# Optimization experiments

Measured on AMD Instinct MI355X. Metric: run time of the kernel, lower is better.

The kernel has to match this reference:

```python
import jax, jax.numpy as jnp
import numpy as np

V, H, B, T = 100000, 512, 4096, 524288
EPS = 1e-5

def setup_inputs() -> dict:
    key = jax.random.key(0)
    ks = jax.random.split(key, 8)
    tokens = jax.random.randint(ks[0], (T,), 0, V, dtype=jnp.int32)
    seg_ids = jnp.sort(jax.random.randint(ks[1], (T,), 0, B, dtype=jnp.int32))
    t = jax.random.bernoulli(ks[2], 0.5, (B,)).astype(jnp.float32)
    emb = jax.random.normal(ks[3], (V, H), dtype=jnp.float32) * 0.1
    W1 = jax.random.normal(ks[4], (H, H), dtype=jnp.float32) * (1.0 / np.sqrt(H))
    b1 = jnp.zeros((H,), jnp.float32)
    gamma = jnp.ones((H,), jnp.float32)
    beta = jnp.zeros((H,), jnp.float32)
    w2 = jax.random.normal(ks[5], (H,), dtype=jnp.float32) * (1.0 / np.sqrt(H))
    b2 = jnp.zeros((), jnp.float32)
    return {"tokens": tokens, "seg_ids": seg_ids, "t": t, "emb": emb,
            "W1": W1, "b1": b1, "gamma": gamma, "beta": beta, "w2": w2, "b2": b2}

def reference(tokens, seg_ids, t, emb, W1, b1, gamma, beta, w2, b2):
    nb = t.shape[0]
    # fused gather + segment-mean (bag-of-words), replaces the per-sample loop
    gathered = emb[tokens]  # [T, H]
    sums = jax.ops.segment_sum(gathered, seg_ids, num_segments=nb)  # [B, H]
    counts = jax.ops.segment_sum(jnp.ones((tokens.shape[0],), jnp.float32), seg_ids, num_segments=nb)
    bow = sums / jnp.maximum(counts, 1.0)[:, None]  # [B, H]
    # Linear -> BatchNorm1d (training-mode batch stats, biased var) -> ReLU
    z = bow @ W1.T + b1  # [B, H]
    mu = jnp.mean(z, axis=0)
    var = jnp.mean((z - mu) ** 2, axis=0)
    zn = (z - mu) * jax.lax.rsqrt(var + EPS) * gamma + beta
    h = jax.nn.relu(zn)  # dropout treated as identity (eval mode) for determinism
    logits = h @ w2 + b2  # [B]
    # BCEWithLogitsLoss: mean(softplus(logit) - t*logit), numerically stable
    loss = jnp.mean(jnp.logaddexp(0.0, logits) - t * logits)
    return (loss, logits)
```

## Files before the change

kernel.cpp:

```cpp
#include <hip/hip_runtime.h>
#include <hip/hip_bf16.h>
#include <hip/hip_fp16.h>
#include <math.h>

constexpr int NTOK = 524288;
constexpr int NB   = 4096;
constexpr int H    = 512;
constexpr float EPS = 1e-5f;

typedef _Float16 half8 __attribute__((ext_vector_type(8)));
typedef float f32x4 __attribute__((ext_vector_type(4)));
struct h4 { __half2 a, b; };

__global__ __launch_bounds__(256) void k_seg_bounds(
    const int* __restrict__ seg, int* __restrict__ bounds) {
  const int i = blockIdx.x * 256 + threadIdx.x;
  const int s = seg[i];
  const int sp = (i == 0) ? -1 : seg[i - 1];
  for (int b = sp + 1; b <= s; ++b) bounds[b] = i;
  if (i == NTOK - 1) {
    for (int b = s + 1; b <= NB; ++b) bounds[b] = NTOK;
  }
}

__global__ __launch_bounds__(256) void k_convert(
    const float* __restrict__ src, h4* __restrict__ dst) {
  size_t i = (size_t)blockIdx.x * 256 + threadIdx.x;
  float4 v = ((const float4*)src)[i];
  h4 o;
  o.a = __floats2half2_rn(v.x, v.y);
  o.b = __floats2half2_rn(v.z, v.w);
  dst[i] = o;
}

__global__ __launch_bounds__(256) void k_gather_mean(
    const int* __restrict__ tokens, const int* __restrict__ bounds,
    const half8* __restrict__ embh, half8* __restrict__ bow_h) {
  const int b = blockIdx.x;
  const int start = bounds[b];
  const int end   = bounds[b + 1];

  const int tid = threadIdx.x;
  const int lane = tid & 63;
  const int g = tid >> 6;

  float acc[8] = {};
  int i = start + g;
  for (; i + 28 < end; i += 32) {
    half8 v0 = embh[(size_t)tokens[i]      * 64 + lane];
    half8 v1 = embh[(size_t)tokens[i + 4]  * 64 + lane];
    half8 v2 = embh[(size_t)tokens[i + 8]  * 64 + lane];
    half8 v3 = embh[(size_t)tokens[i + 12] * 64 + lane];
    half8 v4 = embh[(size_t)tokens[i + 16] * 64 + lane];
    half8 v5 = embh[(size_t)tokens[i + 20] * 64 + lane];
    half8 v6 = embh[(size_t)tokens[i + 24] * 64 + lane];
    half8 v7 = embh[(size_t)tokens[i + 28] * 64 + lane];
#pragma unroll
    for (int j = 0; j < 8; ++j)
      acc[j] += ((float)v0[j] + (float)v1[j]) + ((float)v2[j] + (float)v3[j]) +
                ((float)v4[j] + (float)v5[j]) + ((float)v6[j] + (float)v7[j]);
  }
  for (; i < end; i += 4) {
    half8 v0 = embh[(size_t)tokens[i] * 64 + lane];
#pragma unroll
    for (int j = 0; j < 8; ++j) acc[j] += (float)v0[j];
  }

  __shared__ float part[3][64][9];
  if (g > 0) {
#pragma unroll
    for (int j = 0; j < 8; ++j) part[g - 1][lane][j] = acc[j];
  }
  __syncthreads();
  if (g == 0) {
    const int cnt = end - start;
    const float s = 1.0f / (float)(cnt > 0 ? cnt : 1);
    half8 o;
#pragma unroll
    for (int j = 0; j < 8; ++j) {
      float v = acc[j] + part[0][lane][j] + part[1][lane][j] + part[2][lane][j];
      o[j] = (_Float16)(v * s);
    }
    bow_h[(size_t)b * 64 + lane] = o;
  }
}

__global__ __launch_bounds__(256) void k_gemm_mfma(
    const _Float16* __restrict__ A,
    const _Float16* __restrict__ Bw,
    const float* __restrict__ b1, float* __restrict__ C) {
  const int tid = threadIdx.x;
  const int lane = tid & 63;
  const int gw = blockIdx.x * 4 + (tid >> 6);
  const int m0 = (gw >> 3) * 16;
  const int n0 = (gw & 7) * 64;
  const int l15 = lane & 15, quad = lane >> 4;

  f32x4 acc0 = {}, acc1 = {}, acc2 = {}, acc3 = {};
  const _Float16* ap = A + (size_t)(m0 + l15) * H + quad * 8;
  const _Float16* bp = Bw + (size_t)(n0 + l15) * H + quad * 8;

#pragma unroll
  for (int k = 0; k < H; k += 32) {
    half8 af  = *(const half8*)(ap + k);
    half8 bf0 = *(const half8*)(bp + k);
    half8 bf1 = *(const half8*)(bp + 16 * H + k);
    half8 bf2 = *(const half8*)(bp + 32 * H + k);
    half8 bf3 = *(const half8*)(bp + 48 * H + k);
    acc0 = __builtin_amdgcn_mfma_f32_16x16x32_f16(af, bf0, acc0, 0, 0, 0);
    acc1 = __builtin_amdgcn_mfma_f32_16x16x32_f16(af, bf1, acc1, 0, 0, 0);
    acc2 = __builtin_amdgcn_mfma_f32_16x16x32_f16(af, bf2, acc2, 0, 0, 0);
    acc3 = __builtin_amdgcn_mfma_f32_16x16x32_f16(af, bf3, acc3, 0, 0, 0);
  }

  const float bn0v = b1[n0 + l15];
  const float bn1v = b1[n0 + 16 + l15];
  const float bn2v = b1[n0 + 32 + l15];
  const float bn3v = b1[n0 + 48 + l15];
  float* crow = C + (size_t)(m0 + quad * 4) * H + n0 + l15;
#pragma unroll
  for (int r = 0; r < 4; ++r) {
    crow[(size_t)r * H]      = acc0[r] + bn0v;
    crow[(size_t)r * H + 16] = acc1[r] + bn1v;
    crow[(size_t)r * H + 32] = acc2[r] + bn2v;
    crow[(size_t)r * H + 48] = acc3[r] + bn3v;
  }
}

__global__ __launch_bounds__(256) void k_colstats(
    const float* __restrict__ z, float* __restrict__ ps, float* __restrict__ pss) {
  const int blk = blockIdx.x;
  const int c0 = threadIdx.x * 2;
  const int r0 = blk * 64;
  float s0 = 0, s1 = 0, q0 = 0, q1 = 0;
  for (int r = 0; r < 64; ++r) {
    float2 v = *(const float2*)&z[(size_t)(r0 + r) * H + c0];
    s0 += v.x; s1 += v.y;
    q0 += v.x * v.x; q1 += v.y * v.y;
  }
  ps[blk * H + c0] = s0; ps[blk * H + c0 + 1] = s1;
  pss[blk * H + c0] = q0; pss[blk * H + c0 + 1] = q1;
}

__global__ __launch_bounds__(128) void k_finalize(
    const float* __restrict__ ps, const float* __restrict__ pss,
    const float* __restrict__ gamma, const float* __restrict__ beta,
    float* __restrict__ scale, float* __restrict__ shift,
    float* __restrict__ d_out) {
  const int c = blockIdx.x * 128 + threadIdx.x;
  if (c == 0) d_out[0] = 0.f;
  float s = 0, q = 0;
#pragma unroll 8
  for (int i = 0; i < 64; ++i) { s += ps[i * H + c]; q += pss[i * H + c]; }
  const float mu = s * (1.0f / NB);
  const float var = q * (1.0f / NB) - mu * mu;
  const float rstd = rsqrtf(var + EPS);
  const float sc = rstd * gamma[c];
  scale[c] = sc;
  shift[c] = beta[c] - mu * sc;
}

__global__ __launch_bounds__(256) void k_bn_dot_loss(
    const float* __restrict__ z, const float* __restrict__ scale,
    const float* __restrict__ shift, const float* __restrict__ w2,
    const float* __restrict__ b2, const float* __restrict__ t,
    float* __restrict__ out) {
  const int tid = threadIdx.x;
  const int wave = tid >> 6, lane = tid & 63;
  const int b = blockIdx.x * 4 + wave;
  const float4* __restrict__ z4 = (const float4*)(z + (size_t)b * H);
  const float4* __restrict__ sc4 = (const float4*)scale;
  const float4* __restrict__ sh4 = (const float4*)shift;
  const float4* __restrict__ w24 = (const float4*)w2;
  float acc = 0.f;
#pragma unroll
  for (int i = lane; i < 128; i += 64) {
    float4 zv = z4[i], sc = sc4[i], sh = sh4[i], w = w24[i];
    float h0 = fmaxf(zv.x * sc.x + sh.x, 0.f);
    float h1 = fmaxf(zv.y * sc.y + sh.y, 0.f);
    float h2 = fmaxf(zv.z * sc.z + sh.z, 0.f);
    float h3 = fmaxf(zv.w * sc.w + sh.w, 0.f);
    acc += h0 * w.x + h1 * w.y + h2 * w.z + h3 * w.w;
  }
#pragma unroll
  for (int off = 32; off > 0; off >>= 1) acc += __shfl_down(acc, off, 64);

  __shared__ float lred[4];
  if (lane == 0) {
    const float x = acc + b2[0];
    out[1 + b] = x;
    const float sp = fmaxf(x, 0.f) + log1pf(expf(-fabsf(x)));
    lred[wave] = sp - t[b] * x;
  }
  __syncthreads();
  if (tid == 0) {
    const float ls = (lred[0] + lred[1] + lred[2] + lred[3]) * (1.0f / NB);
    atomicAdd(out, ls);
  }
}

extern "C" void kernel_launch(void* const* d_in, const int* in_sizes, int n_in,
                              void* d_out, int out_size, void* d_ws, size_t ws_size,
                              hipStream_t stream) {
  const int*   tokens = (const int*)d_in[0];
  const int*   seg    = (const int*)d_in[1];
  const float* t      = (const float*)d_in[2];
  const float* emb    = (const float*)d_in[3];
  const float* W1     = (const float*)d_in[4];
  const float* b1     = (const float*)d_in[5];
  const float* gamma  = (const float*)d_in[6];
  const float* beta   = (const float*)d_in[7];
  const float* w2     = (const float*)d_in[8];
  const float* b2     = (const float*)d_in[9];
  float* out = (float*)d_out;

  char* wsb = (char*)d_ws;
  half8*    embh   = (half8*)wsb;
  _Float16* W1h    = (_Float16*)(wsb + 102400000);
  half8*    bow_h  = (half8*)(wsb + 102924288);
  float*    z      = (float*)(wsb + 107118592);
  float*    ps     = (float*)(wsb + 115507200);
  float*    pss    = ps + 64 * H;
  float*    scale  = pss + 64 * H;
  float*    shift  = scale + H;
  int*      bounds = (int*)(shift + H);

  k_seg_bounds<<<NTOK / 256, 256, 0, stream>>>(seg, bounds);
  k_convert<<<50000, 256, 0, stream>>>(emb, (h4*)embh);
  k_convert<<<256, 256, 0, stream>>>(W1, (h4*)W1h);
  k_gather_mean<<<NB, 256, 0, stream>>>(tokens, bounds, embh, bow_h);
  k_gemm_mfma<<<512, 256, 0, stream>>>((const _Float16*)bow_h, W1h, b1, z);
  k_colstats<<<64, 256, 0, stream>>>(z, ps, pss);
  k_finalize<<<4, 128, 0, stream>>>(ps, pss, gamma, beta, scale, shift, out);
  k_bn_dot_loss<<<NB / 4, 256, 0, stream>>>(z, scale, shift, w2, b2, t, out);
}
```

Baseline: 420.5 us.

## Fuse column stats into GEMM epilogue, store z in fp16, shrink gather unroll

```diff
diff --git a/kernel.cpp b/kernel.cpp
--- a/kernel.cpp
+++ b/kernel.cpp
@@ -7,6 +7,7 @@
 constexpr int NB   = 4096;
 constexpr int H    = 512;
 constexpr float EPS = 1e-5f;
+constexpr int MT   = 256;
 
 typedef _Float16 half8 __attribute__((ext_vector_type(8)));
 typedef float f32x4 __attribute__((ext_vector_type(4)));
@@ -46,19 +47,14 @@
 
   float acc[8] = {};
   int i = start + g;
-  for (; i + 28 < end; i += 32) {
+  for (; i + 12 < end; i += 16) {
     half8 v0 = embh[(size_t)tokens[i]      * 64 + lane];
     half8 v1 = embh[(size_t)tokens[i + 4]  * 64 + lane];
     half8 v2 = embh[(size_t)tokens[i + 8]  * 64 + lane];
     half8 v3 = embh[(size_t)tokens[i + 12] * 64 + lane];
-    half8 v4 = embh[(size_t)tokens[i + 16] * 64 + lane];
-    half8 v5 = embh[(size_t)tokens[i + 20] * 64 + lane];
-    half8 v6 = embh[(size_t)tokens[i + 24] * 64 + lane];
-    half8 v7 = embh[(size_t)tokens[i + 28] * 64 + lane];
 #pragma unroll
     for (int j = 0; j < 8; ++j)
-      acc[j] += ((float)v0[j] + (float)v1[j]) + ((float)v2[j] + (float)v3[j]) +
-                ((float)v4[j] + (float)v5[j]) + ((float)v6[j] + (float)v7[j]);
+      acc[j] += ((float)v0[j] + (float)v1[j]) + ((float)v2[j] + (float)v3[j]);
   }
   for (; i < end; i += 4) {
     half8 v0 = embh[(size_t)tokens[i] * 64 + lane];
@@ -88,12 +84,14 @@
 __global__ __launch_bounds__(256) void k_gemm_mfma(
     const _Float16* __restrict__ A,
     const _Float16* __restrict__ Bw,
-    const float* __restrict__ b1, float* __restrict__ C) {
+    const float* __restrict__ b1, _Float16* __restrict__ z_h,
+    float* __restrict__ pps, float* __restrict__ ppq) {
   const int tid = threadIdx.x;
   const int lane = tid & 63;
   const int gw = blockIdx.x * 4 + (tid >> 6);
   const int m0 = (gw >> 3) * 16;
   const int n0 = (gw & 7) * 64;
+  const int mtile = gw >> 3;
   const int l15 = lane & 15, quad = lane >> 4;
 
   f32x4 acc0 = {}, acc1 = {}, acc2 = {}, acc3 = {};
@@ -113,37 +111,30 @@
     acc3 = __builtin_amdgcn_mfma_f32_16x16x32_f16(af, bf3, acc3, 0, 0, 0);
   }
 
-  const float bn0v = b1[n0 + l15];
-  const float bn1v = b1[n0 + 16 + l15];
-  const float bn2v = b1[n0 + 32 + l15];
-  const float bn3v = b1[n0 + 48 + l15];
-  float* crow = C + (size_t)(m0 + quad * 4) * H + n0 + l15;
-#pragma unroll
-  for (int r = 0; r < 4; ++r) {
-    crow[(size_t)r * H]      = acc0[r] + bn0v;
-    crow[(size_t)r * H + 16] = acc1[r] + bn1v;
-    crow[(size_t)r * H + 32] = acc2[r] + bn2v;
-    crow[(size_t)r * H + 48] = acc3[r] + bn3v;
-  }
-}
-
-__global__ __launch_bounds__(256) void k_colstats(
-    const float* __restrict__ z, float* __restrict__ ps, float* __restrict__ pss) {
-  const int blk = blockIdx.x;
-  const int c0 = threadIdx.x * 2;
-  const int r0 = blk * 64;
-  float s0 = 0, s1 = 0, q0 = 0, q1 = 0;
-  for (int r = 0; r < 64; ++r) {
-    float2 v = *(const float2*)&z[(size_t)(r0 + r) * H + c0];
-    s0 += v.x; s1 += v.y;
-    q0 += v.x * v.x; q1 += v.y * v.y;
-  }
-  ps[blk * H + c0] = s0; ps[blk * H + c0 + 1] = s1;
-  pss[blk * H + c0] = q0; pss[blk * H + c0 + 1] = q1;
+  const float bn[4] = { b1[n0 + l15], b1[n0 + 16 + l15],
+                        b1[n0 + 32 + l15], b1[n0 + 48 + l15] };
+  f32x4* accs[4] = { &acc0, &acc1, &acc2, &acc3 };
+  _Float16* zrow = z_h + (size_t)(m0 + quad * 4) * H + n0 + l15;
+#pragma unroll
+  for (int f = 0; f < 4; ++f) {
+    float s = 0.f, q = 0.f;
+#pragma unroll
+    for (int r = 0; r < 4; ++r) {
+      const float v = (*accs[f])[r] + bn[f];
+      zrow[(size_t)r * H + f * 16] = (_Float16)v;
+      s += v; q += v * v;
+    }
+    s += __shfl_xor(s, 16, 64); s += __shfl_xor(s, 32, 64);
+    q += __shfl_xor(q, 16, 64); q += __shfl_xor(q, 32, 64);
+    if (quad == 0) {
+      pps[(size_t)mtile * H + n0 + f * 16 + l15] = s;
+      ppq[(size_t)mtile * H + n0 + f * 16 + l15] = q;
+    }
+  }
 }
 
 __global__ __launch_bounds__(128) void k_finalize(
-    const float* __restrict__ ps, const float* __restrict__ pss,
+    const float* __restrict__ pps, const float* __restrict__ ppq,
     const float* __restrict__ gamma, const float* __restrict__ beta,
     float* __restrict__ scale, float* __restrict__ shift,
     float* __restrict__ d_out) {
@@ -151,7 +142,7 @@
   if (c == 0) d_out[0] = 0.f;
   float s = 0, q = 0;
 #pragma unroll 8
-  for (int i = 0; i < 64; ++i) { s += ps[i * H + c]; q += pss[i * H + c]; }
+  for (int i = 0; i < MT; ++i) { s += pps[(size_t)i * H + c]; q += ppq[(size_t)i * H + c]; }
   const float mu = s * (1.0f / NB);
   const float var = q * (1.0f / NB) - mu * mu;
   const float rstd = rsqrtf(var + EPS);
@@ -161,26 +152,32 @@
 }
 
 __global__ __launch_bounds__(256) void k_bn_dot_loss(
-    const float* __restrict__ z, const float* __restrict__ scale,
+    const _Float16* __restrict__ z_h, const float* __restrict__ scale,
     const float* __restrict__ shift, const float* __restrict__ w2,
     const float* __restrict__ b2, const float* __restrict__ t,
     float* __restrict__ out) {
   const int tid = threadIdx.x;
   const int wave = tid >> 6, lane = tid & 63;
   const int b = blockIdx.x * 4 + wave;
-  const float4* __restrict__ z4 = (const float4*)(z + (size_t)b * H);
-  const float4* __restrict__ sc4 = (const float4*)scale;
-  const float4* __restrict__ sh4 = (const float4*)shift;
-  const float4* __restrict__ w24 = (const float4*)w2;
-  float acc = 0.f;
-#pragma unroll
-  for (int i = lane; i < 128; i += 64) {
-    float4 zv = z4[i], sc = sc4[i], sh = sh4[i], w = w24[i];
-    float h0 = fmaxf(zv.x * sc.x + sh.x, 0.f);
-    float h1 = fmaxf(zv.y * sc.y + sh.y, 0.f);
-    float h2 = fmaxf(zv.z * sc.z + sh.z, 0.f);
-    float h3 = fmaxf(zv.w * sc.w + sh.w, 0.f);
-    acc += h0 * w.x + h1 * w.y + h2 * w.z + h3 * w.w;
+  const half8 zv = ((const half8*)(z_h + (size_t)b * H))[lane];
+  const float4 sc0 = ((const float4*)scale)[lane * 2];
+  const float4 sc1 = ((const float4*)scale)[lane * 2 + 1];
+  const float4 sh0 = ((const float4*)shift)[lane * 2];
+  const float4 sh1 = ((const float4*)shift)[lane * 2 + 1];
+  const float4 w0  = ((const float4*)w2)[lane * 2];
+  const float4 w1  = ((const float4*)w2)[lane * 2 + 1];
+  float acc;
+  {
+    float h0 = fmaxf((float)zv[0] * sc0.x + sh0.x, 0.f);
+    float h1 = fmaxf((float)zv[1] * sc0.y + sh0.y, 0.f);
+    float h2 = fmaxf((float)zv[2] * sc0.z + sh0.z, 0.f);
+    float h3 = fmaxf((float)zv[3] * sc0.w + sh0.w, 0.f);
+    float h4_ = fmaxf((float)zv[4] * sc1.x + sh1.x, 0.f);
+    float h5 = fmaxf((float)zv[5] * sc1.y + sh1.y, 0.f);
+    float h6 = fmaxf((float)zv[6] * sc1.z + sh1.z, 0.f);
+    float h7 = fmaxf((float)zv[7] * sc1.w + sh1.w, 0.f);
+    acc = h0 * w0.x + h1 * w0.y + h2 * w0.z + h3 * w0.w
+        + h4_ * w1.x + h5 * w1.y + h6 * w1.z + h7 * w1.w;
   }
 #pragma unroll
   for (int off = 32; off > 0; off >>= 1) acc += __shfl_down(acc, off, 64);
@@ -218,10 +215,10 @@
   half8*    embh   = (half8*)wsb;
   _Float16* W1h    = (_Float16*)(wsb + 102400000);
   half8*    bow_h  = (half8*)(wsb + 102924288);
-  float*    z      = (float*)(wsb + 107118592);
-  float*    ps     = (float*)(wsb + 115507200);
-  float*    pss    = ps + 64 * H;
-  float*    scale  = pss + 64 * H;
+  _Float16* z_h    = (_Float16*)(wsb + 107118592);
+  float*    pps    = (float*)(wsb + 111312896);
+  float*    ppq    = pps + (size_t)MT * H;
+  float*    scale  = ppq + (size_t)MT * H;
   float*    shift  = scale + H;
   int*      bounds = (int*)(shift + H);
 
@@ -229,8 +226,7 @@
   k_convert<<<50000, 256, 0, stream>>>(emb, (h4*)embh);
   k_convert<<<256, 256, 0, stream>>>(W1, (h4*)W1h);
   k_gather_mean<<<NB, 256, 0, stream>>>(tokens, bounds, embh, bow_h);
-  k_gemm_mfma<<<512, 256, 0, stream>>>((const _Float16*)bow_h, W1h, b1, z);
-  k_colstats<<<64, 256, 0, stream>>>(z, ps, pss);
-  k_finalize<<<4, 128, 0, stream>>>(ps, pss, gamma, beta, scale, shift, out);
-  k_bn_dot_loss<<<NB / 4, 256, 0, stream>>>(z, scale, shift, w2, b2, t, out);
-}
+  k_gemm_mfma<<<512, 256, 0, stream>>>((const _Float16*)bow_h, W1h, b1, z_h, pps, ppq);
+  k_finalize<<<4, 128, 0, stream>>>(pps, ppq, gamma, beta, scale, shift, out);
+  k_bn_dot_loss<<<NB / 4, 256, 0, stream>>>(z_h, scale, shift, w2, b2, t, out);
+}
```

Result: no change. 423.7 us (+0.8%).
